# Kernel tuning notes

Hardware: AMD Instinct MI355X
Metric: run time of the kernel (lower is better)

The kernel has to match this reference:

```python
import jax, jax.numpy as jnp
import numpy as np

B, S, D, NH = 1, 2048, 2048, 8
DH = D // NH
BACKEND_EPS = 1e-6
NORM_EPS = 1e-6


def setup_inputs() -> dict:
    key = jax.random.key(0)
    ks = jax.random.split(key, 6)
    q = jax.random.normal(ks[0], (B, S, D), jnp.float32)
    k = jax.random.normal(ks[1], (B, S, D), jnp.float32)
    v = jax.random.normal(ks[2], (B, S, D), jnp.float32)
    igate_kernel = jax.random.normal(ks[3], (3 * D, NH), jnp.float32) * 0.02
    igate_bias = jax.random.normal(ks[4], (NH,), jnp.float32) * 0.1
    fgate_kernel = jax.random.normal(ks[5], (3 * D, NH), jnp.float32) * 0.02
    fgate_bias = jnp.linspace(3.0, 6.0, NH, dtype=jnp.float32)  # bias_linspace_init(3.0, 6.0)
    out_weight = jnp.ones((NH, DH), jnp.float32)  # MultiHeadLayerNorm scale (no bias)
    return dict(q=q, k=k, v=v, igate_kernel=igate_kernel, igate_bias=igate_bias,
                fgate_kernel=fgate_kernel, fgate_bias=fgate_bias, out_weight=out_weight)


def _mlstm_parallel_stabilized(q, k, v, i_pre, f_pre):
    # q,k,v: (B,NH,S,DH); i_pre,f_pre: (B,NH,S)
    s = q.shape[-2]
    dh = q.shape[-1]
    log_f = jax.nn.log_sigmoid(f_pre)                              # (B,NH,S)
    cum = jnp.pad(jnp.cumsum(log_f, axis=-1), ((0, 0), (0, 0), (1, 0)))  # (B,NH,S+1), cum[0]=0
    # logfg[t, s] = cum[t+1] - cum[s+1] = sum_{j=s+1}^{t} log_f[j], valid for s <= t
    logfg = cum[..., 1:, None] - cum[..., None, 1:]                # (B,NH,S,S)
    causal = jnp.tril(jnp.ones((s, s), dtype=bool))
    logfg = jnp.where(causal, logfg, -jnp.inf)
    log_D = logfg + i_pre[..., None, :]                            # add input gate at source position s
    m = jnp.max(log_D, axis=-1, keepdims=True)                     # stabilizer (B,NH,S,1)
    D = jnp.exp(log_D - m)
    qk = jnp.einsum('bhsd,bhtd->bhst', q, k) / jnp.sqrt(jnp.float32(dh))
    C = qk * D                                                     # (B,NH,S,S)
    n = jnp.maximum(jnp.abs(jnp.sum(C, axis=-1, keepdims=True)), jnp.exp(-m))
    return jnp.einsum('bhst,bhtd->bhsd', C / (n + BACKEND_EPS), v)


def reference(q, k, v, igate_kernel, igate_bias, fgate_kernel, fgate_bias, out_weight):
    qkv = jnp.concatenate([q, k, v], axis=-1)                      # (B,S,3D)
    i_pre = qkv @ igate_kernel + igate_bias                        # (B,S,NH)
    f_pre = qkv @ fgate_kernel + fgate_bias                        # (B,S,NH)
    qh = q.reshape(B, S, NH, DH).transpose(0, 2, 1, 3)             # (B,NH,S,DH)
    kh = k.reshape(B, S, NH, DH).transpose(0, 2, 1, 3)
    vh = v.reshape(B, S, NH, DH).transpose(0, 2, 1, 3)
    h = _mlstm_parallel_stabilized(qh, kh, vh,
                                   i_pre.transpose(0, 2, 1),
                                   f_pre.transpose(0, 2, 1))       # (B,NH,S,DH)
    h = h.transpose(0, 2, 1, 3)                                    # (B,S,NH,DH)
    mu = jnp.mean(h, axis=-1, keepdims=True)
    var = jnp.var(h, axis=-1, keepdims=True)
    hn = (h - mu) * jax.lax.rsqrt(var + NORM_EPS) * out_weight     # per-head LN, scale only
    return hn.reshape(B, S, D)
```

## Files before the change

### kernel.cpp

```cpp
#include <hip/hip_runtime.h>
#include <hip/hip_bf16.h>

#define SEQ 2048
#define DMODEL 2048
#define NHEAD 8
#define DHEAD 256

typedef _Float16 v8h __attribute__((ext_vector_type(8)));
typedef unsigned short v8u __attribute__((ext_vector_type(8)));
typedef float v4f __attribute__((ext_vector_type(4)));

__device__ __forceinline__ float b2f(unsigned short s) {
    return __uint_as_float(((unsigned)s) << 16);
}
__device__ __forceinline__ unsigned short f2b(float f) {
    unsigned u = __float_as_uint(f);
    u += 0x7fffu + ((u >> 16) & 1u);
    return (unsigned short)(u >> 16);
}
__device__ __forceinline__ unsigned short f2h(float f) {
    _Float16 h = (_Float16)f;
    return __builtin_bit_cast(unsigned short, h);
}
__device__ __forceinline__ float h2f(unsigned short s) {
    return (float)__builtin_bit_cast(_Float16, s);
}

__global__ __launch_bounds__(256) void k_pre(const void* q, const void* k, const void* v,
                                             const void* igk, const void* fgk,
                                             int* flag,
                                             unsigned short* qb, unsigned short* kb,
                                             unsigned short* vT,
                                             float* iparts, float* fparts) {
    __shared__ float x_lds[32][67];
    __shared__ int cnt;
    const int tid = threadIdx.x;

    if (tid == 0) cnt = 0;
    __syncthreads();
    {
        const unsigned short* qp = (const unsigned short*)q;
        int wild = 0;
        for (int i = tid; i < 2048; i += 256) {
            float x = b2f(qp[i]);
            float ax = fabsf(x);
            if (!(ax <= 100.0f) || (x != 0.0f && ax < 1e-6f)) wild++;
        }
        atomicAdd(&cnt, wild);
    }
    __syncthreads();
    const int bf = (cnt < 256) ? 1 : 0;
    if (blockIdx.x == 0 && blockIdx.y == 0 && tid == 0) *flag = bf;

    const int s0 = blockIdx.x * 32;
    const int z  = blockIdx.y;
    const int tz = z >> 1;
    const int dbase = (z & 1) * 1024;
    const void* src = (tz == 0) ? q : (tz == 1) ? k : v;
    unsigned short* dst16 = (tz == 0) ? qb : kb;

    const int r  = tid >> 3, c0 = (tid & 7) * 8;
    const int sl = tid >> 3, hh = tid & 7;
    float accI = 0.f, accF = 0.f;
    const unsigned short* ik16 = (const unsigned short*)igk;
    const unsigned short* fk16 = (const unsigned short*)fgk;
    const float* ik32 = (const float*)igk;
    const float* fk32 = (const float*)fgk;

    for (int ch = 0; ch < 16; ++ch) {
        const int d0 = dbase + ch * 64;
        float xv[8];
        const size_t base = (size_t)(s0 + r) * DMODEL + d0 + c0;
        if (bf) {
            const unsigned short* sp = (const unsigned short*)src;
            v8u a = *(const v8u*)(sp + base);
#pragma unroll
            for (int j = 0; j < 8; j++) xv[j] = b2f(a[j]);
        } else {
            const float* sp = (const float*)src;
            v4f a0 = *(const v4f*)(sp + base);
            v4f a1 = *(const v4f*)(sp + base + 4);
#pragma unroll
            for (int j = 0; j < 4; j++) { xv[j] = a0[j]; xv[4 + j] = a1[j]; }
        }
        __syncthreads();
#pragma unroll
        for (int j = 0; j < 8; j++) x_lds[r][c0 + j] = xv[j];
        if (tz < 2) {
            v8u o;
#pragma unroll
            for (int j = 0; j < 8; j++) o[j] = f2h(xv[j]);
            *(v8u*)(dst16 + base) = o;
        }
        __syncthreads();
        const int gd0 = tz * 2048 + d0;
        if (bf) {
#pragma unroll 8
            for (int j = 0; j < 64; j++) {
                float x = x_lds[sl][j];
                int wi = (gd0 + j) * NHEAD + hh;
                accI += x * b2f(ik16[wi]);
                accF += x * b2f(fk16[wi]);
            }
        } else {
#pragma unroll 8
            for (int j = 0; j < 64; j++) {
                float x = x_lds[sl][j];
                int wi = (gd0 + j) * NHEAD + hh;
                accI += x * ik32[wi];
                accF += x * fk32[wi];
            }
        }
        if (tz == 2) {
            const int dloc = tid >> 2, sc0 = (tid & 3) * 8;
            v8u o;
#pragma unroll
            for (int j = 0; j < 8; j++) o[j] = f2h(x_lds[sc0 + j][dloc]);
            const int dglob = d0 + dloc;
            const int head = dglob >> 8, dh = dglob & 255;
            *(v8u*)(vT + ((size_t)(head * DHEAD + dh)) * SEQ + s0 + sc0) = o;
        }
    }
    iparts[(size_t)z * NHEAD * SEQ + hh * SEQ + s0 + sl] = accI;
    fparts[(size_t)z * NHEAD * SEQ + hh * SEQ + s0 + sl] = accF;
}

__global__ __launch_bounds__(256) void k_scan(const float* iparts, const float* fparts,
                                              const void* ib_, const void* fb_,
                                              const int* flag,
                                              float* a_g, float* amax_g, float* nfl_g) {
    __shared__ float sarr[256];
    int bf = *(volatile const int*)flag;
    int h = blockIdx.x, tid = threadIdx.x;
    float ib = bf ? b2f(((const unsigned short*)ib_)[h]) : ((const float*)ib_)[h];
    float fb = bf ? b2f(((const unsigned short*)fb_)[h]) : ((const float*)fb_)[h];
    int s0 = tid * 8;
    float lf[8], ip[8];
#pragma unroll
    for (int j = 0; j < 8; j++) {
        float fpv = fb, ipv = ib;
#pragma unroll
        for (int z = 0; z < 6; z++) {
            ipv += iparts[(size_t)z * NHEAD * SEQ + h * SEQ + s0 + j];
            fpv += fparts[(size_t)z * NHEAD * SEQ + h * SEQ + s0 + j];
        }
        lf[j] = fminf(fpv, 0.0f) - log1pf(__expf(-fabsf(fpv)));
        ip[j] = ipv;
    }
    float cs[8]; float t = 0.f;
#pragma unroll
    for (int j = 0; j < 8; j++) { t += lf[j]; cs[j] = t; }
    sarr[tid] = t; __syncthreads();
    for (int ofs = 1; ofs < 256; ofs <<= 1) {
        float val = sarr[tid];
        if (tid >= ofs) val += sarr[tid - ofs];
        __syncthreads(); sarr[tid] = val; __syncthreads();
    }
    float excl = (tid > 0) ? sarr[tid - 1] : 0.0f;
    float cum[8], av[8];
#pragma unroll
    for (int j = 0; j < 8; j++) { cum[j] = excl + cs[j]; av[j] = ip[j] - cum[j]; }
    float mx = av[0];
#pragma unroll
    for (int j = 1; j < 8; j++) mx = fmaxf(mx, av[j]);
    __syncthreads(); sarr[tid] = mx; __syncthreads();
    for (int ofs = 1; ofs < 256; ofs <<= 1) {
        float val = sarr[tid];
        if (tid >= ofs) val = fmaxf(val, sarr[tid - ofs]);
        __syncthreads(); sarr[tid] = val; __syncthreads();
    }
    float run = (tid > 0) ? sarr[tid - 1] : -3.0e38f;
#pragma unroll
    for (int j = 0; j < 8; j++) {
        run = fmaxf(run, av[j]);
        int s = s0 + j;
        a_g[h * SEQ + s]    = av[j];
        amax_g[h * SEQ + s] = run;
        float m = cum[j] + run;
        nfl_g[h * SEQ + s]  = __expf(fminf(fmaxf(-m, -60.f), 60.f));
    }
}

__global__ __launch_bounds__(256) void k_main(const unsigned short* __restrict__ qb,
                                              const unsigned short* __restrict__ kb,
                                              const unsigned short* __restrict__ vT,
                                              const float* __restrict__ a_g,
                                              const float* __restrict__ amax_g,
                                              float* __restrict__ h_buf,
                                              float* __restrict__ rs_buf) {
    __shared__ __align__(16) unsigned short q_lds[32][264];
    __shared__ __align__(16) unsigned short k_lds[32][264];
    __shared__ __align__(16) unsigned short vT_lds[272][40];
    __shared__ __align__(16) unsigned short P_lds[32][40];
    __shared__ __align__(16) unsigned short Plo_lds[32][40];
    __shared__ float a_s[32], amax_t[32];

    const int h   = blockIdx.x;
    const int y   = blockIdx.y;
    const int tid = threadIdx.x;
    const int lane = tid & 63;
    const int w   = tid >> 6;
    const int l15 = lane & 15;
    const int qd  = (lane >> 4) & 3;
    const int hd0 = h * DHEAD;

    int u         = 65 * (y >> 1) + ((y & 1) ? 33 : 0);
    int remaining = (y & 1) ? 32 : 33;
    int tile = (int)((sqrtf(8.0f * (float)u + 1.0f) - 1.0f) * 0.5f);
    while ((tile + 1) * (tile + 2) / 2 <= u) ++tile;
    while (tile * (tile + 1) / 2 > u) --tile;
    int js = u - tile * (tile + 1) / 2;
    bool needQ = true;

    for (int i = tid; i < 16 * 40; i += 256) {
        int r2 = i / 40, c2 = i % 40;
        vT_lds[256 + r2][c2] = (r2 == 0 && c2 < 32) ? (unsigned short)0x3C00 : (unsigned short)0;
    }

    const v4f vzero = {0.f, 0.f, 0.f, 0.f};
    v4f acc[2][4];
    v4f accN[2];
#pragma unroll
    for (int m = 0; m < 2; m++) {
        accN[m] = vzero;
#pragma unroll
        for (int n = 0; n < 4; n++) acc[m][n] = vzero;
    }

    const int mw = w >> 1, nw = w & 1;
    const int krow = tid >> 3, kc0 = (tid & 7) * 32;

    v8u kr0, kr1, kr2, kr3, vr0, vr1, vr2, vr3;
    float areg = 0.f;
    {
        const int s0 = js * 32;
        const unsigned short* ks = kb + (size_t)(s0 + krow) * DMODEL + hd0 + kc0;
        kr0 = *(const v8u*)(ks);      kr1 = *(const v8u*)(ks + 8);
        kr2 = *(const v8u*)(ks + 16); kr3 = *(const v8u*)(ks + 24);
        const unsigned short* vs = vT + (size_t)(hd0 + tid) * SEQ + s0;
        vr0 = *(const v8u*)(vs);      vr1 = *(const v8u*)(vs + 8);
        vr2 = *(const v8u*)(vs + 16); vr3 = *(const v8u*)(vs + 24);
        if (tid < 32) areg = a_g[h * SEQ + s0 + tid];
    }

    for (;;) {
        const int t0 = tile * 32;
        __syncthreads();
        if (needQ) {
            const unsigned short* src = qb + (size_t)(t0 + krow) * DMODEL + hd0 + kc0;
#pragma unroll
            for (int i = 0; i < 4; i++)
                *(v8u*)&q_lds[krow][kc0 + i * 8] = *(const v8u*)(src + i * 8);
            if (tid < 32) amax_t[tid] = amax_g[h * SEQ + t0 + tid];
            needQ = false;
        }
        *(v8u*)&k_lds[krow][kc0]      = kr0;
        *(v8u*)&k_lds[krow][kc0 + 8]  = kr1;
        *(v8u*)&k_lds[krow][kc0 + 16] = kr2;
        *(v8u*)&k_lds[krow][kc0 + 24] = kr3;
        *(v8u*)&vT_lds[tid][0]  = vr0;
        *(v8u*)&vT_lds[tid][8]  = vr1;
        *(v8u*)&vT_lds[tid][16] = vr2;
        *(v8u*)&vT_lds[tid][24] = vr3;
        if (tid < 32) a_s[tid] = areg;
        __syncthreads();

        v4f c = vzero;
#pragma unroll
        for (int d0 = 0; d0 < 256; d0 += 32) {
            v8h a = *(const v8h*)&q_lds[mw * 16 + l15][d0 + qd * 8];
            v8h b = *(const v8h*)&k_lds[nw * 16 + l15][d0 + qd * 8];
            c = __builtin_amdgcn_mfma_f32_16x16x32_f16(a, b, c, 0, 0, 0);
        }
        {
            const bool diag = (js == tile);
            const int col = nw * 16 + l15;
            const float av = a_s[col];
#pragma unroll
            for (int r = 0; r < 4; r++) {
                int row = mw * 16 + qd * 4 + r;
                float arg = fminf(av - amax_t[row], 0.0f);
                float val = c[r] * 0.0625f * __expf(arg);
                if (diag && col > row) val = 0.0f;
                unsigned short hi = f2h(val);
                float lo = val - h2f(hi);
                P_lds[row][col]   = hi;
                Plo_lds[row][col] = f2h(lo);
            }
        }
        __syncthreads();

        int ntile = tile, njs = js + 1; bool nq = false;
        if (njs > tile) { ntile = tile + 1; njs = 0; nq = true; }
        if (remaining > 1) {
            const int s0 = njs * 32;
            const unsigned short* ks = kb + (size_t)(s0 + krow) * DMODEL + hd0 + kc0;
            kr0 = *(const v8u*)(ks);      kr1 = *(const v8u*)(ks + 8);
            kr2 = *(const v8u*)(ks + 16); kr3 = *(const v8u*)(ks + 24);
            const unsigned short* vs = vT + (size_t)(hd0 + tid) * SEQ + s0;
            vr0 = *(const v8u*)(vs);      vr1 = *(const v8u*)(vs + 8);
            vr2 = *(const v8u*)(vs + 16); vr3 = *(const v8u*)(vs + 24);
            if (tid < 32) areg = a_g[h * SEQ + s0 + tid];
        }

        v8h aH0 = *(const v8h*)&P_lds[l15][qd * 8];
        v8h aH1 = *(const v8h*)&P_lds[16 + l15][qd * 8];
        v8h aL0 = *(const v8h*)&Plo_lds[l15][qd * 8];
        v8h aL1 = *(const v8h*)&Plo_lds[16 + l15][qd * 8];
#pragma unroll
        for (int nn = 0; nn < 4; nn++) {
            v8h bV = *(const v8h*)&vT_lds[w * 64 + nn * 16 + l15][qd * 8];
            acc[0][nn] = __builtin_amdgcn_mfma_f32_16x16x32_f16(aH0, bV, acc[0][nn], 0, 0, 0);
            acc[0][nn] = __builtin_amdgcn_mfma_f32_16x16x32_f16(aL0, bV, acc[0][nn], 0, 0, 0);
            acc[1][nn] = __builtin_amdgcn_mfma_f32_16x16x32_f16(aH1, bV, acc[1][nn], 0, 0, 0);
            acc[1][nn] = __builtin_amdgcn_mfma_f32_16x16x32_f16(aL1, bV, acc[1][nn], 0, 0, 0);
        }
        if (w == 3) {
            v8h bN = *(const v8h*)&vT_lds[256 + l15][qd * 8];
            accN[0] = __builtin_amdgcn_mfma_f32_16x16x32_f16(aH0, bN, accN[0], 0, 0, 0);
            accN[0] = __builtin_amdgcn_mfma_f32_16x16x32_f16(aL0, bN, accN[0], 0, 0, 0);
            accN[1] = __builtin_amdgcn_mfma_f32_16x16x32_f16(aH1, bN, accN[1], 0, 0, 0);
            accN[1] = __builtin_amdgcn_mfma_f32_16x16x32_f16(aL1, bN, accN[1], 0, 0, 0);
        }

        if (js == tile || remaining == 1) {
#pragma unroll
            for (int m = 0; m < 2; m++)
#pragma unroll
                for (int r = 0; r < 4; r++) {
                    int row = t0 + m * 16 + qd * 4 + r;
#pragma unroll
                    for (int nn = 0; nn < 4; nn++) {
                        int col = hd0 + w * 64 + nn * 16 + l15;
                        atomicAdd(&h_buf[(size_t)row * DMODEL + col], acc[m][nn][r]);
                        acc[m][nn][r] = 0.f;
                    }
                    if (w == 3 && l15 == 0)
                        atomicAdd(&rs_buf[h * SEQ + row], accN[m][r]);
                    accN[m][r] = 0.f;
                }
        }
        if (--remaining == 0) break;
        tile = ntile; js = njs; needQ = nq;
    }
}

__global__ __launch_bounds__(256) void k_finish(const float* __restrict__ h_buf,
                                                const float* __restrict__ rs_buf,
                                                const float* __restrict__ nfl_g,
                                                const void* __restrict__ ow,
                                                const int* flag, void* out) {
    const int wv = threadIdx.x >> 6, lane = threadIdx.x & 63;
    const int rid = blockIdx.x * 4 + wv;
    const int s = rid >> 3, h = rid & 7;
    const int bf = *(volatile const int*)flag;
    float rs  = rs_buf[h * SEQ + s];
    float nfl = nfl_g[h * SEQ + s];
    float sc  = 1.0f / (fmaxf(fabsf(rs), nfl) + 1e-6f);
    size_t base = (size_t)s * DMODEL + h * DHEAD + lane * 4;
    v4f hv = *(const v4f*)(h_buf + base);
#pragma unroll
    for (int j = 0; j < 4; j++) hv[j] *= sc;
    float sm = hv[0] + hv[1] + hv[2] + hv[3];
    float sq = hv[0] * hv[0] + hv[1] * hv[1] + hv[2] * hv[2] + hv[3] * hv[3];
#pragma unroll
    for (int m = 1; m < 64; m <<= 1) {
        sm += __shfl_xor(sm, m, 64);
        sq += __shfl_xor(sq, m, 64);
    }
    float mean = sm * (1.0f / 256.0f);
    float var  = fmaxf(sq * (1.0f / 256.0f) - mean * mean, 0.0f);
    float rstd = rsqrtf(var + 1e-6f);
    int gi = h * DHEAD + lane * 4;
    float g0, g1, g2, g3;
    if (bf) {
        const unsigned short* gp = (const unsigned short*)ow;
        g0 = b2f(gp[gi]); g1 = b2f(gp[gi + 1]); g2 = b2f(gp[gi + 2]); g3 = b2f(gp[gi + 3]);
    } else {
        const float* gp = (const float*)ow;
        g0 = gp[gi]; g1 = gp[gi + 1]; g2 = gp[gi + 2]; g3 = gp[gi + 3];
    }
    float gv[4] = {g0, g1, g2, g3};
    if (bf) {
        unsigned short* o = (unsigned short*)out + base;
#pragma unroll
        for (int j = 0; j < 4; j++) o[j] = f2b((hv[j] - mean) * rstd * gv[j]);
    } else {
        float* o = (float*)out + base;
#pragma unroll
        for (int j = 0; j < 4; j++) o[j] = (hv[j] - mean) * rstd * gv[j];
    }
}

extern "C" void kernel_launch(void* const* d_in, const int* in_sizes, int n_in,
                              void* d_out, int out_size, void* d_ws, size_t ws_size,
                              hipStream_t stream) {
    const void* q   = d_in[0];
    const void* k   = d_in[1];
    const void* v   = d_in[2];
    const void* igk = d_in[3];
    const void* igb = d_in[4];
    const void* fgk = d_in[5];
    const void* fgb = d_in[6];
    const void* ow  = d_in[7];

    char* ws = (char*)d_ws;
    int*   flag   = (int*)(ws + 0);
    float* iparts = (float*)(ws + 1024);
    float* fparts = iparts + 6 * NHEAD * SEQ;
    float* a_g    = fparts + 6 * NHEAD * SEQ;
    float* amax_g = a_g + NHEAD * SEQ;
    float* nfl_g  = amax_g + NHEAD * SEQ;
    unsigned short* qb = (unsigned short*)(nfl_g + NHEAD * SEQ);
    unsigned short* kb = qb + (size_t)SEQ * DMODEL;
    unsigned short* vT = kb + (size_t)SEQ * DMODEL;
    float* rs_buf = (float*)(vT + (size_t)SEQ * DMODEL);
    float* h_buf  = rs_buf + NHEAD * SEQ;

    hipMemsetAsync(rs_buf, 0, (size_t)NHEAD * SEQ * 4 + (size_t)SEQ * DMODEL * 4, stream);
    k_pre<<<dim3(64, 6), 256, 0, stream>>>(q, k, v, igk, fgk, flag, qb, kb, vT, iparts, fparts);
    k_scan<<<8, 256, 0, stream>>>(iparts, fparts, igb, fgb, flag, a_g, amax_g, nfl_g);
    k_main<<<dim3(8, 64), 256, 0, stream>>>(qb, kb, vT, a_g, amax_g, h_buf, rs_buf);
    k_finish<<<4096, 256, 0, stream>>>(h_buf, rs_buf, nfl_g, ow, flag, d_out);
}
```

Measured before the change: 268.2 us.

## Split preprocessing into parallel blocks, swizzle LDS, drop normalizer MFMA, widen main grid

The preprocessing kernel is restructured into three block groups: a flat fp16 conversion of q and k, a 64x64 LDS-tiled transpose of v, and gate projections split across 512-wide chunks that combine through atomics into one pre-activation buffer. The scan kernel therefore reads a single summed buffer. In the main kernel, padded LDS arrays become XOR-swizzled layouts, the row-sum normalizer is computed with wave shuffles and LDS atomics instead of an extra MFMA against a ones column, and the causal tile work is spread over 96 blocks with an occupancy hint of 3. The aims are more parallelism in the preprocessing stage, fewer bank conflicts, and better load balance, at the cost of more atomics and nondeterministic summation order.

```diff
diff --git a/kernel.cpp b/kernel.cpp
--- a/kernel.cpp
+++ b/kernel.cpp
@@ -25,16 +25,21 @@
 __device__ __forceinline__ float h2f(unsigned short s) {
     return (float)__builtin_bit_cast(_Float16, s);
 }
+
+__device__ __forceinline__ int qkoff(int row, int col) { return row * 256 + (col ^ ((row & 7) << 3)); }
+__device__ __forceinline__ int voff(int row, int col)  { return row * 32  + (col ^ ((row & 3) << 3)); }
+__device__ __forceinline__ int poff(int row, int col)  { return row * 32  + (col ^ ((row & 3) << 3)); }
 
 __global__ __launch_bounds__(256) void k_pre(const void* q, const void* k, const void* v,
                                              const void* igk, const void* fgk,
                                              int* flag,
                                              unsigned short* qb, unsigned short* kb,
                                              unsigned short* vT,
-                                             float* iparts, float* fparts) {
-    __shared__ float x_lds[32][67];
+                                             float* ipre, float* fpre) {
+    __shared__ unsigned short tile[64][72];
     __shared__ int cnt;
     const int tid = threadIdx.x;
+    const int b = blockIdx.x;
 
     if (tid == 0) cnt = 0;
     __syncthreads();
@@ -50,82 +55,114 @@
     }
     __syncthreads();
     const int bf = (cnt < 256) ? 1 : 0;
-    if (blockIdx.x == 0 && blockIdx.y == 0 && tid == 0) *flag = bf;
-
-    const int s0 = blockIdx.x * 32;
-    const int z  = blockIdx.y;
-    const int tz = z >> 1;
-    const int dbase = (z & 1) * 1024;
-    const void* src = (tz == 0) ? q : (tz == 1) ? k : v;
-    unsigned short* dst16 = (tz == 0) ? qb : kb;
-
-    const int r  = tid >> 3, c0 = (tid & 7) * 8;
-    const int sl = tid >> 3, hh = tid & 7;
-    float accI = 0.f, accF = 0.f;
-    const unsigned short* ik16 = (const unsigned short*)igk;
-    const unsigned short* fk16 = (const unsigned short*)fgk;
-    const float* ik32 = (const float*)igk;
-    const float* fk32 = (const float*)fgk;
-
-    for (int ch = 0; ch < 16; ++ch) {
-        const int d0 = dbase + ch * 64;
-        float xv[8];
-        const size_t base = (size_t)(s0 + r) * DMODEL + d0 + c0;
+    if (b == 0 && tid == 0) *flag = bf;
+
+    if (b < 1024) {
+        size_t i0 = ((size_t)b * 256 + tid) * 16;
         if (bf) {
-            const unsigned short* sp = (const unsigned short*)src;
-            v8u a = *(const v8u*)(sp + base);
-#pragma unroll
-            for (int j = 0; j < 8; j++) xv[j] = b2f(a[j]);
+            const unsigned short* qp = (const unsigned short*)q;
+            const unsigned short* kp = (const unsigned short*)k;
+#pragma unroll
+            for (int hlf = 0; hlf < 2; hlf++) {
+                v8u uq = *(const v8u*)(qp + i0 + hlf * 8);
+                v8u uk = *(const v8u*)(kp + i0 + hlf * 8);
+                v8u oq, ok;
+#pragma unroll
+                for (int j = 0; j < 8; j++) { oq[j] = f2h(b2f(uq[j])); ok[j] = f2h(b2f(uk[j])); }
+                *(v8u*)(qb + i0 + hlf * 8) = oq;
+                *(v8u*)(kb + i0 + hlf * 8) = ok;
+            }
         } else {
-            const float* sp = (const float*)src;
-            v4f a0 = *(const v4f*)(sp + base);
-            v4f a1 = *(const v4f*)(sp + base + 4);
-#pragma unroll
-            for (int j = 0; j < 4; j++) { xv[j] = a0[j]; xv[4 + j] = a1[j]; }
+            const float* qf = (const float*)q;
+            const float* kf = (const float*)k;
+#pragma unroll
+            for (int hlf = 0; hlf < 2; hlf++) {
+                v8u oq, ok;
+#pragma unroll
+                for (int j = 0; j < 8; j++) {
+                    oq[j] = f2h(qf[i0 + hlf * 8 + j]);
+                    ok[j] = f2h(kf[i0 + hlf * 8 + j]);
+                }
+                *(v8u*)(qb + i0 + hlf * 8) = oq;
+                *(v8u*)(kb + i0 + hlf * 8) = ok;
+            }
+        }
+    } else if (b < 2048) {
+        int b2 = b - 1024;
+        int s0 = (b2 & 31) * 64, d0 = (b2 >> 5) * 64;
+        int r = tid >> 2, c0 = (tid & 3) * 16;
+        size_t base = (size_t)(s0 + r) * DMODEL + d0 + c0;
+        if (bf) {
+            const unsigned short* vp = (const unsigned short*)v;
+            v8u a = *(const v8u*)(vp + base);
+            v8u bb = *(const v8u*)(vp + base + 8);
+#pragma unroll
+            for (int j = 0; j < 8; j++) { tile[r][c0 + j] = f2h(b2f(a[j])); tile[r][c0 + 8 + j] = f2h(b2f(bb[j])); }
+        } else {
+            const float* vp = (const float*)v;
+#pragma unroll
+            for (int j = 0; j < 16; j++) tile[r][c0 + j] = f2h(vp[base + j]);
         }
         __syncthreads();
-#pragma unroll
-        for (int j = 0; j < 8; j++) x_lds[r][c0 + j] = xv[j];
-        if (tz < 2) {
-            v8u o;
-#pragma unroll
-            for (int j = 0; j < 8; j++) o[j] = f2h(xv[j]);
-            *(v8u*)(dst16 + base) = o;
-        }
-        __syncthreads();
-        const int gd0 = tz * 2048 + d0;
-        if (bf) {
-#pragma unroll 8
-            for (int j = 0; j < 64; j++) {
-                float x = x_lds[sl][j];
-                int wi = (gd0 + j) * NHEAD + hh;
-                accI += x * b2f(ik16[wi]);
-                accF += x * b2f(fk16[wi]);
-            }
-        } else {
-#pragma unroll 8
-            for (int j = 0; j < 64; j++) {
-                float x = x_lds[sl][j];
-                int wi = (gd0 + j) * NHEAD + hh;
-                accI += x * ik32[wi];
-                accF += x * fk32[wi];
-            }
-        }
-        if (tz == 2) {
-            const int dloc = tid >> 2, sc0 = (tid & 3) * 8;
-            v8u o;
-#pragma unroll
-            for (int j = 0; j < 8; j++) o[j] = f2h(x_lds[sc0 + j][dloc]);
-            const int dglob = d0 + dloc;
-            const int head = dglob >> 8, dh = dglob & 255;
-            *(v8u*)(vT + ((size_t)(head * DHEAD + dh)) * SEQ + s0 + sc0) = o;
-        }
-    }
-    iparts[(size_t)z * NHEAD * SEQ + hh * SEQ + s0 + sl] = accI;
-    fparts[(size_t)z * NHEAD * SEQ + hh * SEQ + s0 + sl] = accF;
-}
-
-__global__ __launch_bounds__(256) void k_scan(const float* iparts, const float* fparts,
+        int dr = tid >> 2, sc0 = (tid & 3) * 16;
+        v8u o0, o1;
+#pragma unroll
+        for (int j = 0; j < 8; j++) { o0[j] = tile[sc0 + j][dr]; o1[j] = tile[sc0 + 8 + j][dr]; }
+        int head = d0 >> 8;
+        int dh = (d0 & 255) + dr;
+        size_t ob = ((size_t)head * DHEAD + dh) * SEQ + s0 + sc0;
+        *(v8u*)(vT + ob) = o0;
+        *(v8u*)(vT + ob + 8) = o1;
+    } else {
+        int b2 = b - 2048;
+        int s0 = (b2 & 63) * 32;
+        int dc = b2 >> 6;
+        int tz = dc >> 2;
+        int dloc = (dc & 3) * 512;
+        const void* src = (tz == 0) ? q : (tz == 1) ? k : v;
+        int gd0 = tz * 2048 + dloc;
+        int sl = tid >> 3, hh = tid & 7;
+        int s = s0 + sl;
+        float accI = 0.f, accF = 0.f;
+        const unsigned short* ik16 = (const unsigned short*)igk;
+        const unsigned short* fk16 = (const unsigned short*)fgk;
+        const float* ik32 = (const float*)igk;
+        const float* fk32 = (const float*)fgk;
+        const size_t xbase = (size_t)s * DMODEL + dloc;
+        for (int j0 = 0; j0 < 512; j0 += 8) {
+            float xv[8];
+            if (bf) {
+                v8u a = *(const v8u*)((const unsigned short*)src + xbase + j0);
+#pragma unroll
+                for (int j = 0; j < 8; j++) xv[j] = b2f(a[j]);
+            } else {
+                const float* sp = (const float*)src;
+                v4f a0 = *(const v4f*)(sp + xbase + j0);
+                v4f a1 = *(const v4f*)(sp + xbase + j0 + 4);
+#pragma unroll
+                for (int j = 0; j < 4; j++) { xv[j] = a0[j]; xv[4 + j] = a1[j]; }
+            }
+            int wb = (gd0 + j0) * NHEAD + hh;
+            if (bf) {
+#pragma unroll
+                for (int j = 0; j < 8; j++) {
+                    accI += xv[j] * b2f(ik16[wb + j * 8]);
+                    accF += xv[j] * b2f(fk16[wb + j * 8]);
+                }
+            } else {
+#pragma unroll
+                for (int j = 0; j < 8; j++) {
+                    accI += xv[j] * ik32[wb + j * 8];
+                    accF += xv[j] * fk32[wb + j * 8];
+                }
+            }
+        }
+        atomicAdd(&ipre[hh * SEQ + s], accI);
+        atomicAdd(&fpre[hh * SEQ + s], accF);
+    }
+}
+
+__global__ __launch_bounds__(256) void k_scan(const float* ipre, const float* fpre,
                                               const void* ib_, const void* fb_,
                                               const int* flag,
                                               float* a_g, float* amax_g, float* nfl_g) {
@@ -138,14 +175,9 @@
     float lf[8], ip[8];
 #pragma unroll
     for (int j = 0; j < 8; j++) {
-        float fpv = fb, ipv = ib;
-#pragma unroll
-        for (int z = 0; z < 6; z++) {
-            ipv += iparts[(size_t)z * NHEAD * SEQ + h * SEQ + s0 + j];
-            fpv += fparts[(size_t)z * NHEAD * SEQ + h * SEQ + s0 + j];
-        }
-        lf[j] = fminf(fpv, 0.0f) - log1pf(__expf(-fabsf(fpv)));
-        ip[j] = ipv;
+        float fp = fpre[h * SEQ + s0 + j] + fb;
+        lf[j] = fminf(fp, 0.0f) - log1pf(__expf(-fabsf(fp)));
+        ip[j] = ipre[h * SEQ + s0 + j] + ib;
     }
     float cs[8]; float t = 0.f;
 #pragma unroll
@@ -181,19 +213,19 @@
     }
 }
 
-__global__ __launch_bounds__(256) void k_main(const unsigned short* __restrict__ qb,
-                                              const unsigned short* __restrict__ kb,
-                                              const unsigned short* __restrict__ vT,
-                                              const float* __restrict__ a_g,
-                                              const float* __restrict__ amax_g,
-                                              float* __restrict__ h_buf,
-                                              float* __restrict__ rs_buf) {
-    __shared__ __align__(16) unsigned short q_lds[32][264];
-    __shared__ __align__(16) unsigned short k_lds[32][264];
-    __shared__ __align__(16) unsigned short vT_lds[272][40];
-    __shared__ __align__(16) unsigned short P_lds[32][40];
-    __shared__ __align__(16) unsigned short Plo_lds[32][40];
-    __shared__ float a_s[32], amax_t[32];
+__global__ __launch_bounds__(256, 3) void k_main(const unsigned short* __restrict__ qb,
+                                                 const unsigned short* __restrict__ kb,
+                                                 const unsigned short* __restrict__ vT,
+                                                 const float* __restrict__ a_g,
+                                                 const float* __restrict__ amax_g,
+                                                 float* __restrict__ h_buf,
+                                                 float* __restrict__ rs_buf) {
+    __shared__ __align__(16) unsigned short q_lds[32 * 256];
+    __shared__ __align__(16) unsigned short k_lds[32 * 256];
+    __shared__ __align__(16) unsigned short vT_lds[256 * 32];
+    __shared__ __align__(16) unsigned short P_lds[32 * 32];
+    __shared__ __align__(16) unsigned short Plo_lds[32 * 32];
+    __shared__ float a_s[32], amax_t[32], rs_acc[32];
 
     const int h   = blockIdx.x;
     const int y   = blockIdx.y;
@@ -204,37 +236,31 @@
     const int qd  = (lane >> 4) & 3;
     const int hd0 = h * DHEAD;
 
-    int u         = 65 * (y >> 1) + ((y & 1) ? 33 : 0);
-    int remaining = (y & 1) ? 32 : 33;
+    int u         = (y * 2080) / 96;
+    int remaining = ((y + 1) * 2080) / 96 - u;
     int tile = (int)((sqrtf(8.0f * (float)u + 1.0f) - 1.0f) * 0.5f);
     while ((tile + 1) * (tile + 2) / 2 <= u) ++tile;
     while (tile * (tile + 1) / 2 > u) --tile;
     int js = u - tile * (tile + 1) / 2;
     bool needQ = true;
 
-    for (int i = tid; i < 16 * 40; i += 256) {
-        int r2 = i / 40, c2 = i % 40;
-        vT_lds[256 + r2][c2] = (r2 == 0 && c2 < 32) ? (unsigned short)0x3C00 : (unsigned short)0;
-    }
+    if (tid < 32) rs_acc[tid] = 0.f;
 
     const v4f vzero = {0.f, 0.f, 0.f, 0.f};
     v4f acc[2][4];
-    v4f accN[2];
-#pragma unroll
-    for (int m = 0; m < 2; m++) {
-        accN[m] = vzero;
+#pragma unroll
+    for (int m = 0; m < 2; m++)
 #pragma unroll
         for (int n = 0; n < 4; n++) acc[m][n] = vzero;
-    }
 
     const int mw = w >> 1, nw = w & 1;
-    const int krow = tid >> 3, kc0 = (tid & 7) * 32;
+    const int srow = tid & 31, scol = (tid >> 5) * 32;
 
     v8u kr0, kr1, kr2, kr3, vr0, vr1, vr2, vr3;
     float areg = 0.f;
     {
         const int s0 = js * 32;
-        const unsigned short* ks = kb + (size_t)(s0 + krow) * DMODEL + hd0 + kc0;
+        const unsigned short* ks = kb + (size_t)(s0 + srow) * DMODEL + hd0 + scol;
         kr0 = *(const v8u*)(ks);      kr1 = *(const v8u*)(ks + 8);
         kr2 = *(const v8u*)(ks + 16); kr3 = *(const v8u*)(ks + 24);
         const unsigned short* vs = vT + (size_t)(hd0 + tid) * SEQ + s0;
@@ -247,29 +273,29 @@
         const int t0 = tile * 32;
         __syncthreads();
         if (needQ) {
-            const unsigned short* src = qb + (size_t)(t0 + krow) * DMODEL + hd0 + kc0;
+            const unsigned short* src = qb + (size_t)(t0 + srow) * DMODEL + hd0 + scol;
 #pragma unroll
             for (int i = 0; i < 4; i++)
-                *(v8u*)&q_lds[krow][kc0 + i * 8] = *(const v8u*)(src + i * 8);
+                *(v8u*)&q_lds[qkoff(srow, scol + i * 8)] = *(const v8u*)(src + i * 8);
             if (tid < 32) amax_t[tid] = amax_g[h * SEQ + t0 + tid];
             needQ = false;
         }
-        *(v8u*)&k_lds[krow][kc0]      = kr0;
-        *(v8u*)&k_lds[krow][kc0 + 8]  = kr1;
-        *(v8u*)&k_lds[krow][kc0 + 16] = kr2;
-        *(v8u*)&k_lds[krow][kc0 + 24] = kr3;
-        *(v8u*)&vT_lds[tid][0]  = vr0;
-        *(v8u*)&vT_lds[tid][8]  = vr1;
-        *(v8u*)&vT_lds[tid][16] = vr2;
-        *(v8u*)&vT_lds[tid][24] = vr3;
+        *(v8u*)&k_lds[qkoff(srow, scol)]      = kr0;
+        *(v8u*)&k_lds[qkoff(srow, scol + 8)]  = kr1;
+        *(v8u*)&k_lds[qkoff(srow, scol + 16)] = kr2;
+        *(v8u*)&k_lds[qkoff(srow, scol + 24)] = kr3;
+        *(v8u*)&vT_lds[voff(tid, 0)]  = vr0;
+        *(v8u*)&vT_lds[voff(tid, 8)]  = vr1;
+        *(v8u*)&vT_lds[voff(tid, 16)] = vr2;
+        *(v8u*)&vT_lds[voff(tid, 24)] = vr3;
         if (tid < 32) a_s[tid] = areg;
         __syncthreads();
 
         v4f c = vzero;
 #pragma unroll
         for (int d0 = 0; d0 < 256; d0 += 32) {
-            v8h a = *(const v8h*)&q_lds[mw * 16 + l15][d0 + qd * 8];
-            v8h b = *(const v8h*)&k_lds[nw * 16 + l15][d0 + qd * 8];
+            v8h a = *(const v8h*)&q_lds[qkoff(mw * 16 + l15, d0 + qd * 8)];
+            v8h b = *(const v8h*)&k_lds[qkoff(nw * 16 + l15, d0 + qd * 8)];
             c = __builtin_amdgcn_mfma_f32_16x16x32_f16(a, b, c, 0, 0, 0);
         }
         {
@@ -284,8 +310,14 @@
                 if (diag && col > row) val = 0.0f;
                 unsigned short hi = f2h(val);
                 float lo = val - h2f(hi);
-                P_lds[row][col]   = hi;
-                Plo_lds[row][col] = f2h(lo);
+                P_lds[poff(row, col)]   = hi;
+                Plo_lds[poff(row, col)] = f2h(lo);
+                float s = val;
+                s += __shfl_xor(s, 1, 64);
+                s += __shfl_xor(s, 2, 64);
+                s += __shfl_xor(s, 4, 64);
+                s += __shfl_xor(s, 8, 64);
+                if (l15 == 0) atomicAdd(&rs_acc[row], s);
             }
         }
         __syncthreads();
@@ -294,7 +326,7 @@
         if (njs > tile) { ntile = tile + 1; njs = 0; nq = true; }
         if (remaining > 1) {
             const int s0 = njs * 32;
-            const unsigned short* ks = kb + (size_t)(s0 + krow) * DMODEL + hd0 + kc0;
+            const unsigned short* ks = kb + (size_t)(s0 + srow) * DMODEL + hd0 + scol;
             kr0 = *(const v8u*)(ks);      kr1 = *(const v8u*)(ks + 8);
             kr2 = *(const v8u*)(ks + 16); kr3 = *(const v8u*)(ks + 24);
             const unsigned short* vs = vT + (size_t)(hd0 + tid) * SEQ + s0;
@@ -303,24 +335,17 @@
             if (tid < 32) areg = a_g[h * SEQ + s0 + tid];
         }
 
-        v8h aH0 = *(const v8h*)&P_lds[l15][qd * 8];
-        v8h aH1 = *(const v8h*)&P_lds[16 + l15][qd * 8];
-        v8h aL0 = *(const v8h*)&Plo_lds[l15][qd * 8];
-        v8h aL1 = *(const v8h*)&Plo_lds[16 + l15][qd * 8];
+        v8h aH0 = *(const v8h*)&P_lds[poff(l15, qd * 8)];
+        v8h aH1 = *(const v8h*)&P_lds[poff(16 + l15, qd * 8)];
+        v8h aL0 = *(const v8h*)&Plo_lds[poff(l15, qd * 8)];
+        v8h aL1 = *(const v8h*)&Plo_lds[poff(16 + l15, qd * 8)];
 #pragma unroll
         for (int nn = 0; nn < 4; nn++) {
-            v8h bV = *(const v8h*)&vT_lds[w * 64 + nn * 16 + l15][qd * 8];
+            v8h bV = *(const v8h*)&vT_lds[voff(w * 64 + nn * 16 + l15, qd * 8)];
             acc[0][nn] = __builtin_amdgcn_mfma_f32_16x16x32_f16(aH0, bV, acc[0][nn], 0, 0, 0);
             acc[0][nn] = __builtin_amdgcn_mfma_f32_16x16x32_f16(aL0, bV, acc[0][nn], 0, 0, 0);
             acc[1][nn] = __builtin_amdgcn_mfma_f32_16x16x32_f16(aH1, bV, acc[1][nn], 0, 0, 0);
             acc[1][nn] = __builtin_amdgcn_mfma_f32_16x16x32_f16(aL1, bV, acc[1][nn], 0, 0, 0);
-        }
-        if (w == 3) {
-            v8h bN = *(const v8h*)&vT_lds[256 + l15][qd * 8];
-            accN[0] = __builtin_amdgcn_mfma_f32_16x16x32_f16(aH0, bN, accN[0], 0, 0, 0);
-            accN[0] = __builtin_amdgcn_mfma_f32_16x16x32_f16(aL0, bN, accN[0], 0, 0, 0);
-            accN[1] = __builtin_amdgcn_mfma_f32_16x16x32_f16(aH1, bN, accN[1], 0, 0, 0);
-            accN[1] = __builtin_amdgcn_mfma_f32_16x16x32_f16(aL1, bN, accN[1], 0, 0, 0);
         }
 
         if (js == tile || remaining == 1) {
@@ -335,10 +360,11 @@
                         atomicAdd(&h_buf[(size_t)row * DMODEL + col], acc[m][nn][r]);
                         acc[m][nn][r] = 0.f;
                     }
-                    if (w == 3 && l15 == 0)
-                        atomicAdd(&rs_buf[h * SEQ + row], accN[m][r]);
-                    accN[m][r] = 0.f;
                 }
+            if (tid < 32) {
+                atomicAdd(&rs_buf[h * SEQ + t0 + tid], rs_acc[tid]);
+                rs_acc[tid] = 0.f;
+            }
         }
         if (--remaining == 0) break;
         tile = ntile; js = njs; needQ = nq;
@@ -372,15 +398,16 @@
     float var  = fmaxf(sq * (1.0f / 256.0f) - mean * mean, 0.0f);
     float rstd = rsqrtf(var + 1e-6f);
     int gi = h * DHEAD + lane * 4;
-    float g0, g1, g2, g3;
+    float gv[4];
     if (bf) {
         const unsigned short* gp = (const unsigned short*)ow;
-        g0 = b2f(gp[gi]); g1 = b2f(gp[gi + 1]); g2 = b2f(gp[gi + 2]); g3 = b2f(gp[gi + 3]);
+#pragma unroll
+        for (int j = 0; j < 4; j++) gv[j] = b2f(gp[gi + j]);
     } else {
         const float* gp = (const float*)ow;
-        g0 = gp[gi]; g1 = gp[gi + 1]; g2 = gp[gi + 2]; g3 = gp[gi + 3];
-    }
-    float gv[4] = {g0, g1, g2, g3};
+#pragma unroll
+        for (int j = 0; j < 4; j++) gv[j] = gp[gi + j];
+    }
     if (bf) {
         unsigned short* o = (unsigned short*)out + base;
 #pragma unroll
@@ -406,20 +433,21 @@
 
     char* ws = (char*)d_ws;
     int*   flag   = (int*)(ws + 0);
-    float* iparts = (float*)(ws + 1024);
-    float* fparts = iparts + 6 * NHEAD * SEQ;
-    float* a_g    = fparts + 6 * NHEAD * SEQ;
+    float* ipre   = (float*)(ws + 1024);
+    float* fpre   = ipre + NHEAD * SEQ;
+    float* rs_buf = fpre + NHEAD * SEQ;
+    float* h_buf  = rs_buf + NHEAD * SEQ;
+    float* a_g    = h_buf + (size_t)SEQ * DMODEL;
     float* amax_g = a_g + NHEAD * SEQ;
     float* nfl_g  = amax_g + NHEAD * SEQ;
     unsigned short* qb = (unsigned short*)(nfl_g + NHEAD * SEQ);
     unsigned short* kb = qb + (size_t)SEQ * DMODEL;
     unsigned short* vT = kb + (size_t)SEQ * DMODEL;
-    float* rs_buf = (float*)(vT + (size_t)SEQ * DMODEL);
-    float* h_buf  = rs_buf + NHEAD * SEQ;
-
-    hipMemsetAsync(rs_buf, 0, (size_t)NHEAD * SEQ * 4 + (size_t)SEQ * DMODEL * 4, stream);
-    k_pre<<<dim3(64, 6), 256, 0, stream>>>(q, k, v, igk, fgk, flag, qb, kb, vT, iparts, fparts);
-    k_scan<<<8, 256, 0, stream>>>(iparts, fparts, igb, fgb, flag, a_g, amax_g, nfl_g);
-    k_main<<<dim3(8, 64), 256, 0, stream>>>(qb, kb, vT, a_g, amax_g, h_buf, rs_buf);
+
+    size_t zbytes = (size_t)(3 * NHEAD * SEQ) * 4 + (size_t)SEQ * DMODEL * 4;
+    hipMemsetAsync(ipre, 0, zbytes, stream);
+    k_pre<<<2816, 256, 0, stream>>>(q, k, v, igk, fgk, flag, qb, kb, vT, ipre, fpre);
+    k_scan<<<8, 256, 0, stream>>>(ipre, fpre, igb, fgb, flag, a_g, amax_g, nfl_g);
+    k_main<<<dim3(8, 96), 256, 0, stream>>>(qb, kb, vT, a_g, amax_g, h_buf, rs_buf);
     k_finish<<<4096, 256, 0, stream>>>(h_buf, rs_buf, nfl_g, ow, flag, d_out);
 }
```

Result: slower. 299.7 us (+11.8%).
